# Kernel optimization log

Measured on AMD Instinct MI355X. Metric: run time of the kernel, lower is better.

Reference implementation:

```python
import jax, jax.numpy as jnp
import numpy as np

EPS = 1e-6


def bbox_ciou(box1, box2):
    # box*: [..., 4] in (cx, cy, w, h); broadcasts like the torch version
    b1_x1, b1_y1 = box1[..., 0] - box1[..., 2] / 2, box1[..., 1] - box1[..., 3] / 2
    b1_x2, b1_y2 = box1[..., 0] + box1[..., 2] / 2, box1[..., 1] + box1[..., 3] / 2
    b2_x1, b2_y1 = box2[..., 0] - box2[..., 2] / 2, box2[..., 1] - box2[..., 3] / 2
    b2_x2, b2_y2 = box2[..., 0] + box2[..., 2] / 2, box2[..., 1] + box2[..., 3] / 2
    inter_w = jnp.clip(jnp.minimum(b1_x2, b2_x2) - jnp.maximum(b1_x1, b2_x1), 0)
    inter_h = jnp.clip(jnp.minimum(b1_y2, b2_y2) - jnp.maximum(b1_y1, b2_y1), 0)
    inter_area = inter_w * inter_h
    b1_area = (b1_x2 - b1_x1) * (b1_y2 - b1_y1)
    b2_area = (b2_x2 - b2_x1) * (b2_y2 - b2_y1)
    union = b1_area + b2_area - inter_area
    iou = inter_area / (union + EPS)
    center_dist = (box1[..., 0] - box2[..., 0]) ** 2 + (box1[..., 1] - box2[..., 1]) ** 2
    enc_w = jnp.maximum(b1_x2, b2_x2) - jnp.minimum(b1_x1, b2_x1)
    enc_h = jnp.maximum(b1_y2, b2_y2) - jnp.minimum(b1_y1, b2_y1)
    enc_diag = enc_w ** 2 + enc_h ** 2
    v = (4.0 / np.pi ** 2) * (jnp.arctan(box1[..., 2] / box1[..., 3])
                              - jnp.arctan(box2[..., 2] / box2[..., 3])) ** 2
    alpha = v / (1 - iou + v + EPS)  # no stop-gradient in the original
    return iou - center_dist / (enc_diag + EPS) - alpha * v


def setup_inputs() -> dict:
    key = jax.random.key(0)
    k1, k2, k3 = jax.random.split(key, 3)
    B, N, D, G, C = 64, 25200, 21, 32, 16
    preds = jax.random.uniform(k1, (B, N, D), dtype=jnp.float32)
    # keep w,h strictly positive (atan(w/h) division) as real box preds would be
    gt_boxes = jax.random.uniform(k2, (B, G, 4), minval=0.05, maxval=1.0, dtype=jnp.float32)
    gt_cls = jax.random.randint(k3, (B, G), 0, C, dtype=jnp.int32)
    return {"preds": preds, "gt_boxes": gt_boxes, "gt_cls": gt_cls}


def reference(preds, gt_boxes, gt_cls):
    lambda_cls, lambda_obj, lambda_box = 1.0, 1.0, 5.0
    # match: CIoU of every pred box vs every GT -> [B, G, N]
    pred_boxes = preds[..., :4]
    ious = bbox_ciou(pred_boxes[:, None, :, :], gt_boxes[:, :, None, :])
    best_idx = jnp.argmax(ious, axis=-1)  # [B, G]
    matched = jnp.take_along_axis(preds, best_idx[..., None], axis=1)  # [B, G, 5+C]
    ciou = bbox_ciou(matched[..., :4], gt_boxes)  # [B, G]
    loss_box = jnp.sum(1.0 - ciou)
    # BCEWithLogits with target 1 on a scalar logit == softplus(-logit)
    loss_obj = jnp.sum(jax.nn.softplus(-matched[..., 4]))
    cls_logit = jnp.take_along_axis(matched[..., 5:], gt_cls[..., None].astype(jnp.int32), axis=-1)[..., 0]
    loss_cls = jnp.sum(jax.nn.softplus(-cls_logit))
    return lambda_box * loss_box + lambda_obj * loss_obj + lambda_cls * loss_cls
```

## Files before the change

### kernel.cpp

```cpp
#include <hip/hip_runtime.h>
#include <math.h>

#ifndef INFINITY
#define INFINITY __builtin_inff()
#endif

#define EPS 1e-6f
#define K4PI2 0.405284734569351086f

constexpr int B = 64;
constexpr int N = 25200;
constexpr int D = 21;
constexpr int G = 32;
constexpr int CHUNKS = 16;
constexpr int CHUNK = N / CHUNKS;
constexpr int BLK = 512;
constexpr int TILE = 512;
constexpr int NW = BLK / 64;
constexpr int STREAMS = NW * 2;
constexpr int NTILES = (CHUNK + TILE - 1) / TILE;

typedef float f32x4u __attribute__((ext_vector_type(4), aligned(4)));

__device__ __forceinline__ float fastrcp(float x) {
    return __builtin_amdgcn_rcpf(x);
}

__device__ __forceinline__ float softplusf(float x) {
    return fmaxf(x, 0.0f) + log1pf(expf(-fabsf(x)));
}

__device__ __forceinline__ float ciou_exact(float p_cx, float p_cy, float pw, float ph,
                                            float g_cx, float g_cy, float gw, float gh) {
    float p_x1 = p_cx - pw * 0.5f, p_y1 = p_cy - ph * 0.5f;
    float p_x2 = p_cx + pw * 0.5f, p_y2 = p_cy + ph * 0.5f;
    float g_x1 = g_cx - gw * 0.5f, g_y1 = g_cy - gh * 0.5f;
    float g_x2 = g_cx + gw * 0.5f, g_y2 = g_cy + gh * 0.5f;
    float iw = fmaxf(fminf(p_x2, g_x2) - fmaxf(p_x1, g_x1), 0.0f);
    float ih = fmaxf(fminf(p_y2, g_y2) - fmaxf(p_y1, g_y1), 0.0f);
    float inter = iw * ih;
    float p_area = (p_x2 - p_x1) * (p_y2 - p_y1);
    float g_area = (g_x2 - g_x1) * (g_y2 - g_y1);
    float uni = p_area + g_area - inter;
    float iou = inter / (uni + EPS);
    float dx = p_cx - g_cx, dy = p_cy - g_cy;
    float cd = dx * dx + dy * dy;
    float ew = fmaxf(p_x2, g_x2) - fminf(p_x1, g_x1);
    float eh = fmaxf(p_y2, g_y2) - fminf(p_y1, g_y1);
    float ed = ew * ew + eh * eh;
    float dat = atanf(pw / ph) - atanf(gw / gh);
    float v = K4PI2 * (dat * dat);
    float alpha = v / (1.0f - iou + v + EPS);
    return iou - cd / (ed + EPS) - alpha * v;
}

__global__ __launch_bounds__(BLK, 6) void k_argmax(const float* __restrict__ preds,
                                                   const float* __restrict__ gt_boxes,
                                                   float* __restrict__ pval,
                                                   int* __restrict__ pidx) {
    __shared__ float4 sP[2][TILE * 2];
    __shared__ float rv[NW][G];
    __shared__ int ri[NW][G];

    const int b = blockIdx.x / CHUNKS;
    const int chunk = blockIdx.x % CHUNKS;
    const int tid = threadIdx.x;
    const int lane = tid & 63;
    const int wid = tid >> 6;
    const int g = lane & 31;
    const int stream = wid * 2 + (lane >> 5);
    const int n0 = chunk * CHUNK;
    const float qnan = __builtin_nanf("");

    const float4 gt4 = *reinterpret_cast<const float4*>(gt_boxes + ((size_t)b * G + g) * 4);
    const float gcx = gt4.x, gcy = gt4.y;
    const float gx1 = gcx - gt4.z * 0.5f, gy1 = gcy - gt4.w * 0.5f;
    const float gx2 = gcx + gt4.z * 0.5f, gy2 = gcy + gt4.w * 0.5f;
    const float garea = (gx2 - gx1) * (gy2 - gy1);
    const float gat = atanf(gt4.z / gt4.w);

    float bestv = -INFINITY;
    int besti = 0x7fffffff;

    {
        const int p = tid;
        if (p < CHUNK) {
            const f32x4u pr =
                *reinterpret_cast<const f32x4u*>(preds + ((size_t)b * N + n0 + p) * D);
            float cx = pr.x, cy = pr.y, w = pr.z, h = pr.w;
            float px1 = cx - w * 0.5f, py1 = cy - h * 0.5f;
            float px2 = cx + w * 0.5f, py2 = cy + h * 0.5f;
            sP[0][2 * tid] = make_float4(px1, py1, px2, py2);
            sP[0][2 * tid + 1] =
                make_float4((px2 - px1) * (py2 - py1) + EPS, atanf(w / h), cx, cy);
        } else {
            sP[0][2 * tid] = make_float4(qnan, qnan, qnan, qnan);
            sP[0][2 * tid + 1] = make_float4(qnan, qnan, qnan, qnan);
        }
    }
    __syncthreads();

    for (int k = 0; k < NTILES; ++k) {
        const int t0 = k * TILE;
        const int buf = k & 1;

        f32x4u raw;
        bool have = false;
        if (k + 1 < NTILES) {
            const int p = t0 + TILE + tid;
            if (p < CHUNK) {
                raw = *reinterpret_cast<const f32x4u*>(preds + ((size_t)b * N + n0 + p) * D);
                have = true;
            }
        }

        const int navail = (CHUNK - t0 < TILE) ? (CHUNK - t0) : TILE;
        const int iters = (navail + STREAMS - 1) / STREAMS;
        const int nbase = n0 + t0;
#pragma unroll 4
        for (int it = 0; it < iters; ++it) {
            const int pp = it * STREAMS + stream;
            const float4 A = sP[buf][2 * pp];
            const float4 Q = sP[buf][2 * pp + 1];
            float iw = fminf(A.z, gx2) - fmaxf(A.x, gx1);
            float ih = fminf(A.w, gy2) - fmaxf(A.y, gy1);
            float inter = fmaxf(iw, 0.0f) * fmaxf(ih, 0.0f);
            float uni = (garea + Q.x) - inter;
            float iou = inter * fastrcp(uni);
            float dx = Q.z - gcx, dy = Q.w - gcy;
            float cd = dx * dx + dy * dy;
            float ew = fmaxf(A.z, gx2) - fminf(A.x, gx1);
            float eh = fmaxf(A.w, gy2) - fminf(A.y, gy1);
            float ed = ew * ew + eh * eh + EPS;
            float dat = Q.y - gat;
            float v = K4PI2 * (dat * dat);
            float den = (1.0f + EPS) + v - iou;
            float ciou = iou - cd * fastrcp(ed) - (v * v) * fastrcp(den);
            if (ciou > bestv) { bestv = ciou; besti = nbase + pp; }
        }

        if (k + 1 < NTILES) {
            const int nb = buf ^ 1;
            if (have) {
                float cx = raw.x, cy = raw.y, w = raw.z, h = raw.w;
                float px1 = cx - w * 0.5f, py1 = cy - h * 0.5f;
                float px2 = cx + w * 0.5f, py2 = cy + h * 0.5f;
                sP[nb][2 * tid] = make_float4(px1, py1, px2, py2);
                sP[nb][2 * tid + 1] =
                    make_float4((px2 - px1) * (py2 - py1) + EPS, atanf(w / h), cx, cy);
            } else {
                sP[nb][2 * tid] = make_float4(qnan, qnan, qnan, qnan);
                sP[nb][2 * tid + 1] = make_float4(qnan, qnan, qnan, qnan);
            }
        }
        __syncthreads();
    }

    {
        float ov = __shfl_down(bestv, 32);
        int oi = __shfl_down(besti, 32);
        if (ov > bestv || (ov == bestv && oi < besti)) { bestv = ov; besti = oi; }
        if (lane < 32) { rv[wid][g] = bestv; ri[wid][g] = besti; }
    }
    __syncthreads();

    if (tid < G) {
        float v = rv[0][tid];
        int i = ri[0][tid];
#pragma unroll
        for (int w = 1; w < NW; ++w) {
            float ov = rv[w][tid];
            int oi = ri[w][tid];
            if (ov > v || (ov == v && oi < i)) { v = ov; i = oi; }
        }
        size_t o = ((size_t)b * G + tid) * CHUNKS + chunk;
        pval[o] = v;
        pidx[o] = i;
    }
}

__global__ __launch_bounds__(64) void k_loss(const float* __restrict__ preds,
                                             const float* __restrict__ gt_boxes,
                                             const int* __restrict__ gt_cls,
                                             const float* __restrict__ pval,
                                             const int* __restrict__ pidx,
                                             float* __restrict__ partial) {
    const int b = blockIdx.x;
    const int tid = threadIdx.x;
    float contrib = 0.0f;
    if (tid < G) {
        const int g = tid;
        size_t base = ((size_t)b * G + g) * CHUNKS;
        float v = pval[base];
        int i = pidx[base];
#pragma unroll
        for (int c = 1; c < CHUNKS; ++c) {
            float ov = pval[base + c];
            int oi = pidx[base + c];
            if (ov > v || (ov == v && oi < i)) { v = ov; i = oi; }
        }
        const float* pr = preds + ((size_t)b * N + i) * D;
        const f32x4u p4 = *reinterpret_cast<const f32x4u*>(pr);
        const float* gb = gt_boxes + ((size_t)b * G + g) * 4;
        float ciou = ciou_exact(p4.x, p4.y, p4.z, p4.w, gb[0], gb[1], gb[2], gb[3]);
        float loss_box = 1.0f - ciou;
        float loss_obj = softplusf(-pr[4]);
        int cls = gt_cls[b * G + g];
        float loss_cls = softplusf(-pr[5 + cls]);
        contrib = 5.0f * loss_box + loss_obj + loss_cls;
    }
#pragma unroll
    for (int off = 32; off > 0; off >>= 1) contrib += __shfl_down(contrib, off);
    if (tid == 0) partial[b] = contrib;
}

__global__ __launch_bounds__(64) void k_final(const float* __restrict__ partial,
                                              float* __restrict__ out) {
    float v = partial[threadIdx.x];
#pragma unroll
    for (int off = 32; off > 0; off >>= 1) v += __shfl_down(v, off);
    if (threadIdx.x == 0) out[0] = v;
}

extern "C" void kernel_launch(void* const* d_in, const int* in_sizes, int n_in,
                              void* d_out, int out_size, void* d_ws, size_t ws_size,
                              hipStream_t stream) {
    const float* preds = (const float*)d_in[0];
    const float* gt_boxes = (const float*)d_in[1];
    const int* gt_cls = (const int*)d_in[2];
    float* out = (float*)d_out;

    float* pval = (float*)d_ws;
    int* pidx = (int*)((char*)d_ws + sizeof(float) * (size_t)B * G * CHUNKS);
    float* partial = (float*)((char*)d_ws + 2 * sizeof(float) * (size_t)B * G * CHUNKS);

    k_argmax<<<B * CHUNKS, BLK, 0, stream>>>(preds, gt_boxes, pval, pidx);
    k_loss<<<B, 64, 0, stream>>>(preds, gt_boxes, gt_cls, pval, pidx, partial);
    k_final<<<1, 64, 0, stream>>>(partial, out);
}
```

Measured before the change: 223.6 us.

## Pack pred pairs into float2 SIMD and merge CIoU divisions into one reciprocal

Changes shared memory from interleaved float4 records to a structure-of-arrays layout, so each lane can load two predictions as float2 vectors and evaluate CIoU on the pair with packed f32 math. The three reciprocals per pair are replaced by one reciprocal of a common denominator, which trades rcp ops for extra multiplies. Launch bounds drop from 6 to 4 waves to give more registers. The common-denominator product can lose precision or overflow, and it changes the rounding that argmax tie-breaking depends on.

```diff
diff --git a/kernel.cpp b/kernel.cpp
--- a/kernel.cpp
+++ b/kernel.cpp
@@ -19,12 +19,16 @@
 constexpr int NW = BLK / 64;
 constexpr int STREAMS = NW * 2;
 constexpr int NTILES = (CHUNK + TILE - 1) / TILE;
-
+constexpr int NF = 8;
+
+typedef float f2 __attribute__((ext_vector_type(2)));
 typedef float f32x4u __attribute__((ext_vector_type(4), aligned(4)));
 
 __device__ __forceinline__ float fastrcp(float x) {
     return __builtin_amdgcn_rcpf(x);
 }
+__device__ __forceinline__ f2 vmin2(f2 a, f2 b) { return __builtin_elementwise_min(a, b); }
+__device__ __forceinline__ f2 vmax2(f2 a, f2 b) { return __builtin_elementwise_max(a, b); }
 
 __device__ __forceinline__ float softplusf(float x) {
     return fmaxf(x, 0.0f) + log1pf(expf(-fabsf(x)));
@@ -54,11 +58,11 @@
     return iou - cd / (ed + EPS) - alpha * v;
 }
 
-__global__ __launch_bounds__(BLK, 6) void k_argmax(const float* __restrict__ preds,
+__global__ __launch_bounds__(BLK, 4) void k_argmax(const float* __restrict__ preds,
                                                    const float* __restrict__ gt_boxes,
                                                    float* __restrict__ pval,
                                                    int* __restrict__ pidx) {
-    __shared__ float4 sP[2][TILE * 2];
+    __shared__ float sF[2][NF][TILE];
     __shared__ float rv[NW][G];
     __shared__ int ri[NW][G];
 
@@ -78,6 +82,12 @@
     const float gx2 = gcx + gt4.z * 0.5f, gy2 = gcy + gt4.w * 0.5f;
     const float garea = (gx2 - gx1) * (gy2 - gy1);
     const float gat = atanf(gt4.z / gt4.w);
+    const f2 gx1s = {gx1, gx1}, gy1s = {gy1, gy1}, gx2s = {gx2, gx2}, gy2s = {gy2, gy2};
+    const f2 gcxs = {gcx, gcx}, gcys = {gcy, gcy}, gareas = {garea, garea};
+    const f2 gats = {gat, gat};
+    const f2 zs = {0.0f, 0.0f}, epss = {EPS, EPS};
+    const f2 k4s = {K4PI2, K4PI2};
+    const f2 opes = {1.0f + EPS, 1.0f + EPS};
 
     float bestv = -INFINITY;
     int besti = 0x7fffffff;
@@ -90,12 +100,13 @@
             float cx = pr.x, cy = pr.y, w = pr.z, h = pr.w;
             float px1 = cx - w * 0.5f, py1 = cy - h * 0.5f;
             float px2 = cx + w * 0.5f, py2 = cy + h * 0.5f;
-            sP[0][2 * tid] = make_float4(px1, py1, px2, py2);
-            sP[0][2 * tid + 1] =
-                make_float4((px2 - px1) * (py2 - py1) + EPS, atanf(w / h), cx, cy);
+            sF[0][0][p] = px1; sF[0][1][p] = py1; sF[0][2][p] = px2; sF[0][3][p] = py2;
+            sF[0][4][p] = cx;  sF[0][5][p] = cy;
+            sF[0][6][p] = (px2 - px1) * (py2 - py1) + EPS;
+            sF[0][7][p] = atanf(w / h);
         } else {
-            sP[0][2 * tid] = make_float4(qnan, qnan, qnan, qnan);
-            sP[0][2 * tid + 1] = make_float4(qnan, qnan, qnan, qnan);
+#pragma unroll
+            for (int f = 0; f < NF; ++f) sF[0][f][p] = qnan;
         }
     }
     __syncthreads();
@@ -115,42 +126,61 @@
         }
 
         const int navail = (CHUNK - t0 < TILE) ? (CHUNK - t0) : TILE;
-        const int iters = (navail + STREAMS - 1) / STREAMS;
+        const int npairs = (navail + 1) >> 1;
+        const int iters = (npairs + STREAMS - 1) / STREAMS;
         const int nbase = n0 + t0;
 #pragma unroll 4
         for (int it = 0; it < iters; ++it) {
-            const int pp = it * STREAMS + stream;
-            const float4 A = sP[buf][2 * pp];
-            const float4 Q = sP[buf][2 * pp + 1];
-            float iw = fminf(A.z, gx2) - fmaxf(A.x, gx1);
-            float ih = fminf(A.w, gy2) - fmaxf(A.y, gy1);
-            float inter = fmaxf(iw, 0.0f) * fmaxf(ih, 0.0f);
-            float uni = (garea + Q.x) - inter;
-            float iou = inter * fastrcp(uni);
-            float dx = Q.z - gcx, dy = Q.w - gcy;
-            float cd = dx * dx + dy * dy;
-            float ew = fmaxf(A.z, gx2) - fminf(A.x, gx1);
-            float eh = fmaxf(A.w, gy2) - fminf(A.y, gy1);
-            float ed = ew * ew + eh * eh + EPS;
-            float dat = Q.y - gat;
-            float v = K4PI2 * (dat * dat);
-            float den = (1.0f + EPS) + v - iou;
-            float ciou = iou - cd * fastrcp(ed) - (v * v) * fastrcp(den);
-            if (ciou > bestv) { bestv = ciou; besti = nbase + pp; }
+            const int q = it * STREAMS + stream;
+            const int e = 2 * q;
+            const f2 px1 = *(const f2*)&sF[buf][0][e];
+            const f2 py1 = *(const f2*)&sF[buf][1][e];
+            const f2 px2 = *(const f2*)&sF[buf][2][e];
+            const f2 py2 = *(const f2*)&sF[buf][3][e];
+            const f2 pcx = *(const f2*)&sF[buf][4][e];
+            const f2 pcy = *(const f2*)&sF[buf][5][e];
+            const f2 pae = *(const f2*)&sF[buf][6][e];
+            const f2 pat = *(const f2*)&sF[buf][7][e];
+
+            f2 iw = vmin2(px2, gx2s) - vmax2(px1, gx1s);
+            f2 ih = vmin2(py2, gy2s) - vmax2(py1, gy1s);
+            f2 I = vmax2(iw, zs) * vmax2(ih, zs);
+            f2 U = (pae + gareas) - I;
+            f2 dx = pcx - gcxs, dy = pcy - gcys;
+            f2 cd = dx * dx + dy * dy;
+            f2 ew = vmax2(px2, gx2s) - vmin2(px1, gx1s);
+            f2 eh = vmax2(py2, gy2s) - vmin2(py1, gy1s);
+            f2 ed = ew * ew + eh * eh + epss;
+            f2 dat = pat - gats;
+            f2 v = k4s * (dat * dat);
+            f2 D2 = (opes + v) * U - I;
+            f2 v2 = v * v;
+            f2 edD2 = ed * D2;
+            f2 Ued = U * ed;
+            f2 UD2 = U * D2;
+            f2 denom = Ued * D2;
+            f2 numer = I * edD2 - cd * UD2 - v2 * Ued;
+
+            float c0 = numer.x * fastrcp(denom.x);
+            float c1 = numer.y * fastrcp(denom.y);
+            if (c0 > bestv) { bestv = c0; besti = nbase + e; }
+            if (c1 > bestv) { bestv = c1; besti = nbase + e + 1; }
         }
 
         if (k + 1 < NTILES) {
             const int nb = buf ^ 1;
+            const int p = tid;
             if (have) {
                 float cx = raw.x, cy = raw.y, w = raw.z, h = raw.w;
                 float px1 = cx - w * 0.5f, py1 = cy - h * 0.5f;
                 float px2 = cx + w * 0.5f, py2 = cy + h * 0.5f;
-                sP[nb][2 * tid] = make_float4(px1, py1, px2, py2);
-                sP[nb][2 * tid + 1] =
-                    make_float4((px2 - px1) * (py2 - py1) + EPS, atanf(w / h), cx, cy);
+                sF[nb][0][p] = px1; sF[nb][1][p] = py1; sF[nb][2][p] = px2; sF[nb][3][p] = py2;
+                sF[nb][4][p] = cx;  sF[nb][5][p] = cy;
+                sF[nb][6][p] = (px2 - px1) * (py2 - py1) + EPS;
+                sF[nb][7][p] = atanf(w / h);
             } else {
-                sP[nb][2 * tid] = make_float4(qnan, qnan, qnan, qnan);
-                sP[nb][2 * tid + 1] = make_float4(qnan, qnan, qnan, qnan);
+#pragma unroll
+                for (int f = 0; f < NF; ++f) sF[nb][f][p] = qnan;
             }
         }
         __syncthreads();
```

Result: faster. 214.8 us (-3.9%).
